# Kernel tuning notes

Measured on AMD Instinct MI355X. Metric: run time of the kernel, lower is better.

## Reference

```python
import jax, jax.numpy as jnp
import numpy as np

N_BLOCKS = 16
N_FEATS = 64
SCALE = 2
RGB_RANGE = 255.0
RGB_MEAN = np.array([0.4488, 0.4371, 0.4040], dtype=np.float32)  # DIV2K mean used by EDSR MeanShift


def conv2d(x, w, b=None):
    # x: [N,C,H,W], w: [O,I,kh,kw], SAME padding, stride 1
    y = jax.lax.conv_general_dilated(x, w, (1, 1), 'SAME',
                                     dimension_numbers=('NCHW', 'OIHW', 'NCHW'))
    if b is not None:
        y = y + b[None, :, None, None]
    return y


def ste_sign(x):
    # sign with straight-through estimator (identity gradient)
    return x + jax.lax.stop_gradient(jnp.sign(x) - x)


def bin_conv(x, w):
    # XNOR-style 1-bit conv: binarize activations to {-1,+1} (sign, STE),
    # binarize weights to sign(w) * alpha where alpha = per-output-channel mean(|w|).
    xb = ste_sign(x)
    alpha = jnp.mean(jnp.abs(w), axis=(1, 2, 3), keepdims=True)  # [O,1,1,1]
    wb = ste_sign(w) * alpha
    return conv2d(xb, wb)


def pixel_shuffle(x, r):
    # torch nn.PixelShuffle semantics
    n, c, h, w = x.shape
    x = x.reshape(n, c // (r * r), r, r, h, w)
    x = x.transpose(0, 1, 4, 2, 5, 3)  # [n, c', h, r, w, r]
    return x.reshape(n, c // (r * r), h * r, w * r)


def setup_inputs() -> dict:
    key = jax.random.key(0)
    ks = jax.random.split(key, 8)
    fan = 1.0 / np.sqrt(N_FEATS * 9)
    x = jax.random.uniform(ks[0], (16, 3, 128, 128), jnp.float32) * RGB_RANGE
    w_head = jax.random.normal(ks[1], (N_FEATS, 3, 3, 3), jnp.float32) * (1.0 / np.sqrt(3 * 9))
    w_body = jax.random.normal(ks[2], (N_BLOCKS, 2, N_FEATS, N_FEATS, 3, 3), jnp.float32) * fan
    w_body_last = jax.random.normal(ks[3], (N_FEATS, N_FEATS, 3, 3), jnp.float32) * fan
    w_up = jax.random.normal(ks[4], (N_FEATS * SCALE * SCALE, N_FEATS, 3, 3), jnp.float32) * fan
    w_tail = jax.random.normal(ks[5], (3, N_FEATS, 3, 3), jnp.float32) * fan
    b_tail = jnp.zeros((3,), jnp.float32)
    return {'x': x, 'w_head': w_head, 'w_body': w_body, 'w_body_last': w_body_last,
            'w_up': w_up, 'w_tail': w_tail, 'b_tail': b_tail}


def reference(x, w_head, w_body, w_body_last, w_up, w_tail, b_tail):
    shift = jnp.asarray(RGB_RANGE * RGB_MEAN).reshape(1, 3, 1, 1)
    x = x - shift                      # sub_mean
    h = conv2d(x, w_head)              # full-precision head, [N,64,H,W]
    r = h
    for i in range(N_BLOCKS):          # fixed layer count
        t = bin_conv(r, w_body[i, 0])
        t = jnp.tanh(t)
        t = bin_conv(t, w_body[i, 1])
        r = r + t                      # res_scale = 1
    r = bin_conv(r, w_body_last)
    res = r + h                        # global skip; this is `out`
    t = conv2d(res, w_up)              # 64 -> 64*r^2
    t = pixel_shuffle(t, SCALE)        # [N,64,H*r,W*r]
    t = conv2d(t, w_tail, b_tail)      # 64 -> 3
    out_img = t + shift                # add_mean
    return (out_img, res)
```

## Files before the change

### kernel.cpp

```cpp
#include <hip/hip_runtime.h>
#include <stdint.h>

typedef unsigned long long u64;
typedef unsigned int u32;
typedef _Float16 f16;
using i32x4  = __attribute__((ext_vector_type(4))) int;
using i32x16 = __attribute__((ext_vector_type(16))) int;
using f32x4  = __attribute__((ext_vector_type(4))) float;
using f16x4  = __attribute__((ext_vector_type(4))) _Float16;

#define HW 16384

#define OFF_R      0ull
#define OFF_SG0    67108864ull
#define OFF_SG1    69206016ull
#define OFF_NZT    71303168ull
#define OFF_WBSG   73400320ull
#define OFF_ALPHA  74616832ull
#define OFF_WEFF   74625280ull

__global__ __launch_bounds__(256) void k_prep_wbsg(const float* __restrict__ wbody, const float* __restrict__ wlast,
                                                   signed char* __restrict__ wB, float* __restrict__ alpha){
  int t = blockIdx.x*256 + threadIdx.x;
  if (t >= 33*9*64) return;
  int o = t & 63, tap = (t>>6)%9, cid = t/(64*9);
  const float* src = (cid < 32) ? (wbody + (size_t)cid*36864) : wlast;
  u32 d[16];
  #pragma unroll
  for (int c4=0;c4<16;c4++){
    u32 v=0;
    #pragma unroll
    for (int j=0;j<4;j++){
      float w = src[(o*64 + c4*4+j)*9 + tap];
      v |= ((w < 0.f) ? 0xFFu : 0x01u) << (8*j);
    }
    d[c4]=v;
  }
  i32x4* dst = (i32x4*)(wB + ((size_t)(cid*9+tap)*64 + o)*64);
  #pragma unroll
  for (int k=0;k<4;k++){ i32x4 v; v[0]=(int)d[4*k]; v[1]=(int)d[4*k+1]; v[2]=(int)d[4*k+2]; v[3]=(int)d[4*k+3]; dst[k]=v; }
  if (tap==0){
    float s=0.f;
    for (int ci=0;ci<64;ci++)
      #pragma unroll
      for (int tp=0;tp<9;tp++) s += fabsf(src[(o*64+ci)*9+tp]);
    alpha[cid*64+o] = s * (1.0f/576.0f);
  }
}

__global__ __launch_bounds__(256) void k_prep_weff(const float* __restrict__ wup, const float* __restrict__ wtail,
                                                   float* __restrict__ weff){
  int idx = blockIdx.x*256 + threadIdx.x;
  int rx = idx & 3;
  int px = (idx >> 2) & 1;
  int base = idx >> 3;
  int o  = base % 3;
  int t2 = base / 3;
  int ci = t2 & 63;
  int ry = (t2 >> 6) & 3;
  int py = (t2 >> 8) & 1;
  int e  = t2 >> 9;
  int ex = e % 3, ey = e / 3;
  int ry_off = (py - 2) + ry;
  int rx_off = (px - 2) + rx;
  float acc = 0.f;
  for (int dy=0; dy<3; dy++){
    if (ey==1 && dy==0) continue;
    if (ey==2 && dy==2) continue;
    int pydy = py + dy - 1;
    int sy = ((pydy + 4) >> 1) - 2;
    int vy = (pydy + 4) & 1;
    int a = ry_off + 1 - sy;
    if (a < 0 || a > 2) continue;
    for (int dx=0; dx<3; dx++){
      if (ex==0 && dx==0) continue;
      if (ex==2 && dx==2) continue;
      int pxdx = px + dx - 1;
      int sx = ((pxdx + 4) >> 1) - 2;
      int vx = (pxdx + 4) & 1;
      int b = rx_off + 1 - sx;
      if (b < 0 || b > 2) continue;
      for (int c=0; c<64; c++){
        int u = c*4 + vy*2 + vx;
        acc += wtail[((o*64+c)*3+dy)*3+dx] * wup[((u*64+ci)*3+a)*3+b];
      }
    }
  }
  weff[idx] = acc;
}

__global__ __launch_bounds__(256) void k_head(const float* __restrict__ x, const float* __restrict__ wh,
                                              f16* __restrict__ r, float* __restrict__ h, u64* __restrict__ sgR){
  __shared__ float wl[64*27];
  for (int j=threadIdx.x; j<64*27; j+=256) wl[j] = wh[j];
  __syncthreads();
  const int id = blockIdx.x*256 + threadIdx.x;
  const int n = id >> 14, p = id & 16383;
  const int yy = p >> 7, xx = p & 127;
  float xv[27];
  const float sh[3] = {114.444f, 111.4605f, 103.02f};
  #pragma unroll
  for (int tap=0; tap<9; tap++){
    int Yq = yy + tap/3 - 1, Xq = xx + tap%3 - 1;
    bool v = ((unsigned)Yq < 128u) && ((unsigned)Xq < 128u);
    int q = (Yq << 7) + Xq;
    #pragma unroll
    for (int c=0; c<3; c++)
      xv[c*9+tap] = v ? (x[(size_t)(n*3+c)*HW + q] - sh[c]) : 0.f;
  }
  u64 sg = 0;
  for (int o=0; o<64; o++){
    float acc = 0.f;
    #pragma unroll
    for (int j=0; j<27; j++) acc += wl[o*27+j] * xv[j];
    f16 rv = (f16)acc;
    r[(size_t)(n*64+o)*HW + p] = rv;
    h[(size_t)(n*64+o)*HW + p] = acc;
    sg |= (u64)((float)rv < 0.f) << o;
  }
  sgR[id] = sg;
}

template<int MODE>
__global__ __launch_bounds__(256) void k_bconv(const u64* __restrict__ sgIn, const u64* __restrict__ nzIn,
                                               const signed char* __restrict__ wB, const float* __restrict__ alphaC,
                                               f16* __restrict__ rbuf, u64* __restrict__ sgOut,
                                               u64* __restrict__ nzOut, float* __restrict__ resbuf){
  __shared__ signed char Abytes[4*68*80];

  const int bx = blockIdx.x;
  const int n  = bx >> 7;
  const int rem = bx & 127;
  const int y0 = (rem >> 1) << 1;
  const int x0 = (rem & 1) << 6;

  const int lane = threadIdx.x & 63;
  const int wid  = threadIdx.x >> 6;
  const int rrow = wid >> 1;
  const int och  = wid & 1;
  const int nn   = lane & 31;
  const int q    = lane >> 5;

  i32x4 Bf[9][2];
  #pragma unroll
  for (int t=0;t<9;t++)
    #pragma unroll
    for (int h=0;h<2;h++)
      Bf[t][h] = *(const i32x4*)(wB + ((size_t)(t*64 + och*32 + nn))*64 + h*32 + q*16);

  for (int s = threadIdx.x; s < 4*66; s += 256){
    int g = s/66, c = s%66;
    int y = y0 + g - 1, xcol = x0 + c - 1;
    u64 pos=0, neg=0;
    if (((unsigned)y < 128u) && ((unsigned)xcol < 128u)){
      int p = (n<<14) + (y<<7) + xcol;
      u64 sg = sgIn[p];
      if (MODE==1){ u64 nz = nzIn[p]; pos = nz & ~sg; neg = nz & sg; }
      else        { pos = ~sg;        neg = sg; }
    }
    u32 plo=(u32)pos, phi=(u32)(pos>>32), nlo=(u32)neg, nhi=(u32)(neg>>32);
    u32 tmp[16];
    #pragma unroll
    for (int i=0;i<16;i++){
      u32 np = ((i<8) ? (plo >> (4*i)) : (phi >> (4*i-32))) & 0xFu;
      u32 nm = ((i<8) ? (nlo >> (4*i)) : (nhi >> (4*i-32))) & 0xFu;
      u32 bp = (np * 0x00204081u) & 0x01010101u;
      u32 bn = (nm * 0x00204081u) & 0x01010101u;
      tmp[i] = bp | (bn * 0xFFu);
    }
    i32x4* dst = (i32x4*)&Abytes[(g*68 + c)*80];
    #pragma unroll
    for (int k=0;k<4;k++){ i32x4 v; v[0]=(int)tmp[4*k]; v[1]=(int)tmp[4*k+1]; v[2]=(int)tmp[4*k+2]; v[3]=(int)tmp[4*k+3]; dst[k]=v; }
  }
  __syncthreads();

  const float al = (MODE==0) ? 0.f : alphaC[och*32 + nn];

  for (int xh=0; xh<2; xh++){
    i32x16 acc;
    #pragma unroll
    for (int k=0;k<16;k++) acc[k]=0;

    const i32x4* Ap = (const i32x4*)&Abytes[(rrow*68 + xh*32 + nn)*80 + q*16];
    #pragma unroll
    for (int dy=0;dy<3;dy++)
      #pragma unroll
      for (int dx=0;dx<3;dx++){
        const int t = dy*3+dx;
        #pragma unroll
        for (int h=0;h<2;h++){
          i32x4 a = Ap[(dy*68+dx)*5 + h*2];
          acc = __builtin_amdgcn_mfma_i32_32x32x32_i8(a, Bf[t][h], acc, 0, 0, 0);
        }
      }

    const int ybase = y0 + rrow, xbase = x0 + xh*32;

    if (MODE==0){
      u32 sgc=0, nzc=0;
      #pragma unroll
      for (int reg=0; reg<16; reg++){
        u64 bs = __ballot(acc[reg] < 0);
        u64 bn = __ballot(acc[reg] != 0);
        const int px0 = (reg&3) + ((reg>>2)<<3);
        sgc = (lane==px0  ) ? (u32)bs       : sgc;
        sgc = (lane==px0+4) ? (u32)(bs>>32) : sgc;
        nzc = (lane==px0  ) ? (u32)bn       : nzc;
        nzc = (lane==px0+4) ? (u32)(bn>>32) : nzc;
      }
      if (lane < 32){
        int p = (n<<14) + (ybase<<7) + xbase + lane;
        ((u32*)sgOut)[p*2 + och] = sgc;
        ((u32*)nzOut)[p*2 + och] = nzc;
      }
    } else if (MODE==1){
      float newr[16];
      f16* rp = rbuf + ((size_t)((n<<6) + och*32 + nn))*HW + (ybase<<7) + xbase;
      #pragma unroll
      for (int k2=0;k2<4;k2++){
        f16x4 rv4 = *(f16x4*)(rp + 4*q + 8*k2);
        #pragma unroll
        for (int j=0;j<4;j++){
          float rv = (float)rv4[j] + al * (float)acc[4*k2+j];
          rv4[j] = (f16)rv;
          newr[4*k2+j] = (float)rv4[j];
        }
        *(f16x4*)(rp + 4*q + 8*k2) = rv4;
      }
      u32 sgc=0;
      #pragma unroll
      for (int reg=0; reg<16; reg++){
        u64 b = __ballot(newr[reg] < 0.f);
        const int px0 = (reg&3) + ((reg>>2)<<3);
        sgc = (lane==px0  ) ? (u32)b       : sgc;
        sgc = (lane==px0+4) ? (u32)(b>>32) : sgc;
      }
      if (lane < 32){
        int p = (n<<14) + (ybase<<7) + xbase + lane;
        ((u32*)sgOut)[p*2 + och] = sgc;
      }
    } else {
      float* hp = resbuf + ((size_t)((n<<6) + och*32 + nn))*HW + (ybase<<7) + xbase;
      #pragma unroll
      for (int k2=0;k2<4;k2++){
        f32x4 hv = *(f32x4*)(hp + 4*q + 8*k2);
        #pragma unroll
        for (int j=0;j<4;j++) hv[j] += al * (float)acc[4*k2+j];
        *(f32x4*)(hp + 4*q + 8*k2) = hv;
      }
    }
  }
}

__global__ __launch_bounds__(128) void k_tail(const float* __restrict__ res, const float* __restrict__ weff,
                                              const float* __restrict__ btail, float* __restrict__ out){
  const int id = blockIdx.x;
  const int xcd = id & 7;
  const int l = id >> 3;
  const int n = xcd*2 + (l & 1);
  const int Y = l >> 1;
  const int x = threadIdx.x;
  const int py = Y & 1, y = Y >> 1;
  const int ey = (Y==0) ? 1 : ((Y==255) ? 2 : 0);
  const float* Ws = weff + (size_t)(((ey*3+1)*2+py)) * 6144;
  float acc[3][2] = {{0.f,0.f},{0.f,0.f},{0.f,0.f}};
  for (int ry=0; ry<4; ry++){
    const int yy = y + (py-2) + ry;
    const bool rowv = ((unsigned)yy < 128u);
    const float* Wr = Ws + ry*1536;
    const float* rp = res + (size_t)n*64*HW + yy*128 + x;
    for (int ci=0; ci<64; ci++){
      const float* pp = rp + (size_t)ci*HW;
      float v[5];
      #pragma unroll
      for (int j=0; j<5; j++){
        int xxc = x - 2 + j;
        v[j] = (rowv && (unsigned)xxc < 128u) ? pp[j-2] : 0.f;
      }
      const float* Wc = Wr + ci*24;
      #pragma unroll
      for (int o=0; o<3; o++)
        #pragma unroll
        for (int px=0; px<2; px++)
          #pragma unroll
          for (int rx=0; rx<4; rx++)
            acc[o][px] += Wc[(o*2+px)*4+rx] * v[px+rx];
    }
  }
  const float sh[3] = {114.444f, 111.4605f, 103.02f};
  #pragma unroll
  for (int o=0; o<3; o++){
    #pragma unroll
    for (int px=0; px<2; px++){
      int X = 2*x + px;
      if (X == 0 || X == 255) continue;
      out[(size_t)((n*3+o)*256+Y)*256 + X] = acc[o][px] + btail[o] + sh[o];
    }
  }
}

__global__ __launch_bounds__(256) void k_border(const float* __restrict__ res, const float* __restrict__ weff,
                                                const float* __restrict__ btail, float* __restrict__ out){
  int t = blockIdx.x*256 + threadIdx.x;
  if (t >= 8192) return;
  int side = t & 1;
  int Y = (t >> 1) & 255;
  int n = t >> 9;
  int X = side ? 255 : 0;
  int px = side, x = side ? 127 : 0;
  int py = Y & 1, y = Y >> 1;
  int ey = (Y==0) ? 1 : ((Y==255) ? 2 : 0);
  int ex = side ? 2 : 0;
  const float* Ws = weff + (size_t)((ey*3+ex)*2+py) * 6144;
  float acc[3] = {0.f,0.f,0.f};
  for (int ry=0; ry<4; ry++){
    int yy = y + (py-2) + ry;
    bool rowv = ((unsigned)yy < 128u);
    const float* rp = res + (size_t)n*64*HW + yy*128;
    for (int ci=0; ci<64; ci++){
      const float* Wc = Ws + ry*1536 + ci*24 + px*4;
      #pragma unroll
      for (int rx=0; rx<4; rx++){
        int xxc = x + (px-2) + rx;
        float v = (rowv && (unsigned)xxc < 128u) ? rp[(size_t)ci*HW + xxc] : 0.f;
        acc[0] += Wc[0*8+rx] * v;
        acc[1] += Wc[1*8+rx] * v;
        acc[2] += Wc[2*8+rx] * v;
      }
    }
  }
  const float sh[3] = {114.444f, 111.4605f, 103.02f};
  for (int o=0; o<3; o++)
    out[(size_t)((n*3+o)*256+Y)*256 + X] = acc[o] + btail[o] + sh[o];
}

extern "C" void kernel_launch(void* const* d_in, const int* in_sizes, int n_in,
                              void* d_out, int out_size, void* d_ws, size_t ws_size,
                              hipStream_t stream) {
  const float* x      = (const float*)d_in[0];
  const float* w_head = (const float*)d_in[1];
  const float* w_body = (const float*)d_in[2];
  const float* w_last = (const float*)d_in[3];
  const float* w_up   = (const float*)d_in[4];
  const float* w_tail = (const float*)d_in[5];
  const float* b_tail = (const float*)d_in[6];

  char* ws = (char*)d_ws;
  f16*  r      = (f16*) (ws + OFF_R);
  u64*  sg0    = (u64*) (ws + OFF_SG0);
  u64*  sg1    = (u64*) (ws + OFF_SG1);
  u64*  nzT    = (u64*) (ws + OFF_NZT);
  signed char* wBsg = (signed char*)(ws + OFF_WBSG);
  float* alpha = (float*)(ws + OFF_ALPHA);
  float* weff  = (float*)(ws + OFF_WEFF);

  float* out = (float*)d_out;
  float* res = out + 3145728;

  k_prep_wbsg<<<75, 256, 0, stream>>>(w_body, w_last, wBsg, alpha);
  k_prep_weff<<<432, 256, 0, stream>>>(w_up, w_tail, weff);
  k_head<<<1024, 256, 0, stream>>>(x, w_head, r, res, sg0);
  for (int i=0; i<16; i++){
    k_bconv<0><<<2048, 256, 0, stream>>>(sg0, nullptr, wBsg + (size_t)(2*i)*36864,
                                         nullptr, nullptr, sg1, nzT, nullptr);
    k_bconv<1><<<2048, 256, 0, stream>>>(sg1, nzT, wBsg + (size_t)(2*i+1)*36864,
                                         alpha + (2*i+1)*64, r, sg0, nullptr, nullptr);
  }
  k_bconv<2><<<2048, 256, 0, stream>>>(sg0, nullptr, wBsg + (size_t)32*36864,
                                       alpha + 32*64, nullptr, nullptr, nullptr, res);
  k_tail<<<4096, 128, 0, stream>>>(res, weff, b_tail, out);
  k_border<<<32, 256, 0, stream>>>(res, weff, b_tail, out);
}
```

Baseline: 1.299 ms.

## Restructure tail conv to compute four output rows per block with split-channel reduction

The fused upsample+tail kernel now has each thread compute four output row pairs from a 7-row input window, so loaded activations are reused across rows. It also splits the 64 input channels across two half-blocks and reduces the partial sums through shared memory. Weights are repacked into an interleaved layout so packed float2 FMAs can be used, and output stores become vectorised. The interior kernel now writes the top and bottom border rows too, so the border kernel is widened to recompute those rows. This adds a repack kernel and some overwriting of border outputs.

Measured after the change: 1.610 ms. +23.9%, slower.

```diff
diff --git a/kernel.cpp b/kernel.cpp
--- a/kernel.cpp
+++ b/kernel.cpp
@@ -6,12 +6,14 @@
 typedef _Float16 f16;
 using i32x4  = __attribute__((ext_vector_type(4))) int;
 using i32x16 = __attribute__((ext_vector_type(16))) int;
+using f32x2  = __attribute__((ext_vector_type(2))) float;
 using f32x4  = __attribute__((ext_vector_type(4))) float;
 using f16x4  = __attribute__((ext_vector_type(4))) _Float16;
 
 #define HW 16384
 
 #define OFF_R      0ull
+#define OFF_WEFF2  35651584ull
 #define OFF_SG0    67108864ull
 #define OFF_SG1    69206016ull
 #define OFF_NZT    71303168ull
@@ -89,6 +91,18 @@
   weff[idx] = acc;
 }
 
+__global__ __launch_bounds__(256) void k_prep_repack(const float* __restrict__ weff, float* __restrict__ w2){
+  int t = blockIdx.x*256 + threadIdx.x;
+  int px = t & 1;
+  int q  = t >> 1;
+  int rx = q & 3;  q >>= 2;
+  int o  = q % 3;  q /= 3;
+  int ry = q & 3;  q >>= 2;
+  int ci = q & 63;
+  int py = q >> 6;
+  w2[t] = weff[(size_t)(2+py)*6144 + ry*1536 + ci*24 + (o*2+px)*4 + rx];
+}
+
 __global__ __launch_bounds__(256) void k_head(const float* __restrict__ x, const float* __restrict__ wh,
                                               f16* __restrict__ r, float* __restrict__ h, u64* __restrict__ sgR){
   __shared__ float wl[64*27];
@@ -252,49 +266,91 @@
   }
 }
 
-__global__ __launch_bounds__(128) void k_tail(const float* __restrict__ res, const float* __restrict__ weff,
-                                              const float* __restrict__ btail, float* __restrict__ out){
-  const int id = blockIdx.x;
+__global__ __launch_bounds__(256,4) void k_tail(const float* __restrict__ res, const float* __restrict__ w2,
+                                                const float* __restrict__ btail, float* __restrict__ out){
+  __shared__ f32x2 red[128][13];
+  const int id  = blockIdx.x;
   const int xcd = id & 7;
-  const int l = id >> 3;
-  const int n = xcd*2 + (l & 1);
-  const int Y = l >> 1;
-  const int x = threadIdx.x;
-  const int py = Y & 1, y = Y >> 1;
-  const int ey = (Y==0) ? 1 : ((Y==255) ? 2 : 0);
-  const float* Ws = weff + (size_t)(((ey*3+1)*2+py)) * 6144;
-  float acc[3][2] = {{0.f,0.f},{0.f,0.f},{0.f,0.f}};
-  for (int ry=0; ry<4; ry++){
-    const int yy = y + (py-2) + ry;
-    const bool rowv = ((unsigned)yy < 128u);
-    const float* Wr = Ws + ry*1536;
-    const float* rp = res + (size_t)n*64*HW + yy*128 + x;
-    for (int ci=0; ci<64; ci++){
-      const float* pp = rp + (size_t)ci*HW;
-      float v[5];
-      #pragma unroll
-      for (int j=0; j<5; j++){
-        int xxc = x - 2 + j;
-        v[j] = (rowv && (unsigned)xxc < 128u) ? pp[j-2] : 0.f;
-      }
-      const float* Wc = Wr + ci*24;
-      #pragma unroll
-      for (int o=0; o<3; o++)
-        #pragma unroll
-        for (int px=0; px<2; px++)
+  const int t   = id >> 3;
+  const int n   = xcd*2 + (t & 1);
+  const int py  = (t >> 1) & 1;
+  const int yg  = t >> 2;
+  const int y0  = yg << 2;
+  const int x   = threadIdx.x & 127;
+  const int ch  = threadIdx.x >> 7;
+  const int rbase = y0 + py - 2;
+
+  int xo[5]; float cm[5];
+  #pragma unroll
+  for (int j=0;j<5;j++){
+    int c = x - 2 + j;
+    cm[j] = ((unsigned)c < 128u) ? 1.f : 0.f;
+    xo[j] = c < 0 ? 0 : (c > 127 ? 127 : c);
+  }
+
+  f32x2 acc[4][3];
+  #pragma unroll
+  for (int k=0;k<4;k++)
+    #pragma unroll
+    for (int o=0;o<3;o++) acc[k][o] = (f32x2)(0.f);
+
+  const float* rbn = res + (size_t)n*64*HW;
+  const int ci0 = ch*32;
+  #pragma unroll 1
+  for (int ci=ci0; ci<ci0+32; ci++){
+    const float* rp = rbn + (size_t)ci*HW;
+    float v[7][5];
+    #pragma unroll
+    for (int w=0;w<7;w++){
+      const int row = rbase + w;
+      if ((unsigned)row < 128u){
+        const float* q = rp + (row<<7);
+        #pragma unroll
+        for (int j=0;j<5;j++) v[w][j] = q[xo[j]] * cm[j];
+      } else {
+        #pragma unroll
+        for (int j=0;j<5;j++) v[w][j] = 0.f;
+      }
+    }
+    const float* wp = w2 + (size_t)(py*64 + ci)*96;
+    #pragma unroll
+    for (int k=0;k<4;k++){
+      #pragma unroll
+      for (int ry=0;ry<4;ry++){
+        const int w = k + ry;
+        const float* wr = wp + ry*24;
+        #pragma unroll
+        for (int o=0;o<3;o++){
           #pragma unroll
-          for (int rx=0; rx<4; rx++)
-            acc[o][px] += Wc[(o*2+px)*4+rx] * v[px+rx];
-    }
-  }
-  const float sh[3] = {114.444f, 111.4605f, 103.02f};
-  #pragma unroll
-  for (int o=0; o<3; o++){
-    #pragma unroll
-    for (int px=0; px<2; px++){
-      int X = 2*x + px;
-      if (X == 0 || X == 255) continue;
-      out[(size_t)((n*3+o)*256+Y)*256 + X] = acc[o][px] + btail[o] + sh[o];
+          for (int rx=0;rx<4;rx++){
+            f32x2 wv = *(const f32x2*)(wr + (o*4+rx)*2);
+            f32x2 vp; vp[0] = v[w][rx]; vp[1] = v[w][rx+1];
+            acc[k][o] = __builtin_elementwise_fma(wv, vp, acc[k][o]);
+          }
+        }
+      }
+    }
+  }
+
+  if (ch==1){
+    #pragma unroll
+    for (int k=0;k<4;k++)
+      #pragma unroll
+      for (int o=0;o<3;o++) red[x][k*3+o] = acc[k][o];
+  }
+  __syncthreads();
+  if (ch==0){
+    const float sh[3] = {114.444f, 111.4605f, 103.02f};
+    #pragma unroll
+    for (int k=0;k<4;k++){
+      const int Y = ((y0 + k) << 1) + py;
+      #pragma unroll
+      for (int o=0;o<3;o++){
+        f32x2 s2 = acc[k][o] + red[x][k*3+o];
+        const float b = btail[o] + sh[o];
+        s2[0] += b; s2[1] += b;
+        *(f32x2*)(out + (((size_t)((n*3+o)*256 + Y)) << 8) + 2*x) = s2;
+      }
     }
   }
 }
@@ -302,15 +358,20 @@
 __global__ __launch_bounds__(256) void k_border(const float* __restrict__ res, const float* __restrict__ weff,
                                                 const float* __restrict__ btail, float* __restrict__ out){
   int t = blockIdx.x*256 + threadIdx.x;
-  if (t >= 8192) return;
-  int side = t & 1;
-  int Y = (t >> 1) & 255;
-  int n = t >> 9;
-  int X = side ? 255 : 0;
-  int px = side, x = side ? 127 : 0;
+  if (t >= 16384) return;
+  int n    = t >> 10;
+  int rem  = t & 1023;
+  int edge = rem >> 8;
+  int pos  = rem & 255;
+  int X, Y;
+  if (edge==0){ Y = 0;   X = pos; if (X==0 || X==255) return; }
+  else if (edge==1){ Y = 255; X = pos; if (X==0 || X==255) return; }
+  else if (edge==2){ X = 0;   Y = pos; }
+  else            { X = 255; Y = pos; }
+  int px = X & 1, x = X >> 1;
   int py = Y & 1, y = Y >> 1;
   int ey = (Y==0) ? 1 : ((Y==255) ? 2 : 0);
-  int ex = side ? 2 : 0;
+  int ex = (X==0) ? 0 : ((X==255) ? 2 : 1);
   const float* Ws = weff + (size_t)((ey*3+ex)*2+py) * 6144;
   float acc[3] = {0.f,0.f,0.f};
   for (int ry=0; ry<4; ry++){
@@ -353,12 +414,14 @@
   signed char* wBsg = (signed char*)(ws + OFF_WBSG);
   float* alpha = (float*)(ws + OFF_ALPHA);
   float* weff  = (float*)(ws + OFF_WEFF);
+  float* weff2 = (float*)(ws + OFF_WEFF2);
 
   float* out = (float*)d_out;
   float* res = out + 3145728;
 
   k_prep_wbsg<<<75, 256, 0, stream>>>(w_body, w_last, wBsg, alpha);
   k_prep_weff<<<432, 256, 0, stream>>>(w_up, w_tail, weff);
+  k_prep_repack<<<48, 256, 0, stream>>>(weff, weff2);
   k_head<<<1024, 256, 0, stream>>>(x, w_head, r, res, sg0);
   for (int i=0; i<16; i++){
     k_bconv<0><<<2048, 256, 0, stream>>>(sg0, nullptr, wBsg + (size_t)(2*i)*36864,
@@ -368,6 +431,6 @@
   }
   k_bconv<2><<<2048, 256, 0, stream>>>(sg0, nullptr, wBsg + (size_t)32*36864,
                                        alpha + 32*64, nullptr, nullptr, nullptr, res);
-  k_tail<<<4096, 128, 0, stream>>>(res, weff, b_tail, out);
-  k_border<<<32, 256, 0, stream>>>(res, weff, b_tail, out);
-}
+  k_tail<<<1024, 256, 0, stream>>>(res, weff2, b_tail, out);
+  k_border<<<64, 256, 0, stream>>>(res, weff, b_tail, out);
+}
```
